# Kernel tuning notes

Hardware: AMD Instinct MI355X
Metric: run time of the kernel (lower is better)

The kernel has to match this reference:

```python
import jax, jax.numpy as jnp
import numpy as np

V, E, H = 50000, 128, 256  # vocab, embedding_size, hidden_size
S, B = 512, 64             # seq_len, batch (seq-first, torch LSTM default)


def setup_inputs() -> dict:
    key = jax.random.key(0)
    ks = jax.random.split(key, 10)
    u = 1.0 / np.sqrt(H)  # torch LSTM/Linear init bound

    def unif(k, sh):
        return jax.random.uniform(k, sh, jnp.float32, -u, u)

    emb = jax.random.normal(ks[0], (V, E), jnp.float32) * 0.02
    emb = emb.at[0].set(0.0)  # padding_idx=0

    inp = {
        "seq": jax.random.randint(ks[1], (S, B), 0, V),
        "emb": emb,
        # forward direction weights (gate order i,f,g,o like torch)
        "W_ih_f": unif(ks[2], (4 * H, E)),
        "W_hh_f": unif(ks[3], (4 * H, H)),
        "b_f": unif(ks[4], (4 * H,)),  # b_ih + b_hh fused (identical math)
        # reverse direction
        "W_ih_b": unif(ks[5], (4 * H, E)),
        "W_hh_b": unif(ks[6], (4 * H, H)),
        "b_b": unif(ks[7], (4 * H,)),
        # classification head over concatenated bi-directional features
        "W_out": unif(ks[8], (1, 2 * H)),
        "b_out": unif(ks[9], (1,)),
    }
    return inp


def _lstm_scan(xg, W_hh):
    """xg: [S,B,4H] precomputed input-gate projections; returns hidden seq [S,B,H]."""
    b = xg.shape[1]
    h0 = jnp.zeros((b, H), xg.dtype)
    c0 = jnp.zeros((b, H), xg.dtype)

    def step(carry, xg_t):
        h, c = carry
        gates = xg_t + h @ W_hh.T  # [B,4H]
        i, f, g, o = jnp.split(gates, 4, axis=-1)
        i = jax.nn.sigmoid(i)
        f = jax.nn.sigmoid(f)
        g = jnp.tanh(g)
        o = jax.nn.sigmoid(o)
        c = f * c + i * g
        h = o * jnp.tanh(c)
        return (h, c), h

    _, hs = jax.lax.scan(step, (h0, c0), xg)
    return hs


def reference(seq, emb, W_ih_f, W_hh_f, b_f, W_ih_b, W_hh_b, b_b, W_out, b_out):
    # embedding with padding_idx=0 (row 0 contributes zero)
    x = jnp.where((seq == 0)[..., None], 0.0, emb[seq])  # [S,B,E]

    xg_f = jnp.einsum("sbe,ge->sbg", x, W_ih_f) + b_f          # [S,B,4H]
    hs_f = _lstm_scan(xg_f, W_hh_f)                             # [S,B,H]

    xr = x[::-1]
    xg_b = jnp.einsum("sbe,ge->sbg", xr, W_ih_b) + b_b
    hs_b = _lstm_scan(xg_b, W_hh_b)[::-1]                       # [S,B,H]

    out = jnp.concatenate([hs_f, hs_b], axis=-1)                # [S,B,2H]
    last = out[-1]                                              # [B,2H]
    return jax.nn.sigmoid(last @ W_out.T + b_out)               # [B,1]
```

## Files before the change

kernel.cpp:

```cpp
#include <hip/hip_runtime.h>
#include <hip/hip_bf16.h>
#include <stdint.h>
#include <string.h>

#define S_LEN 512
#define NBATCH 64
#define EDIM 128
#define HDIM 256
#define GDIM 1024

#define WQ_SCALE 1024.0f
#define HQ_SCALE 127.0f
#define DEQ_SCALE (1.0f / 130048.0f)

typedef __attribute__((ext_vector_type(8))) short short8;
typedef __attribute__((ext_vector_type(4))) short short4v;
typedef __attribute__((ext_vector_type(4))) float float4v;
typedef __attribute__((ext_vector_type(4))) int int4v;

#define OFF_WHH8 0u
#define SZ_WHH8 (256u * 64u * 16u)
#define OFF_WIH (OFF_WHH8 + SZ_WHH8)
#define SZ_WIH (64u * 4u * 64u * 16u)
#define OFF_XG ((size_t)(OFF_WIH + SZ_WIH))
#define SZ_XG ((size_t)S_LEN * NBATCH * GDIM * 2)
#define OFF_HF (OFF_XG + SZ_XG)

__device__ __forceinline__ short f2bf(float f) {
    union { float f; unsigned u; } v;
    v.f = f;
    unsigned r = (v.u + 0x7fffu + ((v.u >> 16) & 1u)) >> 16;
    return (short)r;
}
__device__ __forceinline__ float bf2f(short s) {
    union { unsigned u; float f; } v;
    v.u = ((unsigned)(unsigned short)s) << 16;
    return v.f;
}
__device__ __forceinline__ float sigm(float x) {
    float e = __expf(-x);
    return __builtin_amdgcn_rcpf(1.0f + e);
}
__device__ __forceinline__ float tanh_(float x) {
    float e = __expf(2.0f * x);
    return 1.0f - 2.0f * __builtin_amdgcn_rcpf(e + 1.0f);
}

__global__ __launch_bounds__(256) void prep_frags(const float* __restrict__ src,
                                                  char* __restrict__ dst,
                                                  int K, int nchunks, int nfrags) {
    int id = blockIdx.x * blockDim.x + threadIdx.x;
    int lane = id & 63;
    int f = id >> 6;
    if (f >= nfrags) return;
    int tile = f / nchunks;
    int c = f - tile * nchunks;
    int row = tile * 16 + (lane & 15);
    int k0 = c * 32 + ((lane >> 4) * 8);
    const float* s = src + (size_t)row * K + k0;
    short8 pack;
#pragma unroll
    for (int j = 0; j < 8; ++j) pack[j] = f2bf(s[j]);
    *(short8*)(dst + ((size_t)f * 64 + lane) * 16) = pack;
}

__global__ __launch_bounds__(256) void prep_whh_i8(const float* __restrict__ src,
                                                   char* __restrict__ dst) {
    int id = blockIdx.x * blockDim.x + threadIdx.x;
    int lane = id & 63;
    int f = id >> 6;
    int tile = f >> 2, kc = f & 3;
    int row = tile * 16 + (lane & 15);
    int k0 = kc * 64 + ((lane >> 4) * 16);
    const float* s = src + (size_t)row * HDIM + k0;
    union { char b[16]; int4v v; } u;
#pragma unroll
    for (int b = 0; b < 16; ++b)
        u.b[b] = (char)(int)rintf(s[b] * WQ_SCALE);
    *(int4v*)(dst + ((size_t)f * 64 + lane) * 16) = u.v;
}

__global__ __launch_bounds__(256) void input_proj(const int* __restrict__ seq,
                                                  const float* __restrict__ emb,
                                                  const char* __restrict__ wih_frags,
                                                  const float* __restrict__ bias,
                                                  char* __restrict__ xg) {
    __shared__ __align__(16) short lx[4][16][136];
    int tid = threadIdx.x;
    int t0 = blockIdx.x * 4;
    int g = blockIdx.y;

    {
        int row = tid >> 2;
        int tt = row >> 4, m = row & 15;
        int k0 = (tid & 3) * 32;
        int v = seq[(t0 + tt) * NBATCH + g * 16 + m];
        const float* src = emb + (size_t)v * EDIM + k0;
        bool zero = (v == 0);
#pragma unroll
        for (int u = 0; u < 32; u += 4) {
            float4v f = *(const float4v*)(src + u);
            short4v p;
#pragma unroll
            for (int e = 0; e < 4; ++e) p[e] = zero ? (short)0 : f2bf(f[e]);
            *(short4v*)&lx[tt][m][k0 + u] = p;
        }
    }
    __syncthreads();

    int lane = tid & 63, w = tid >> 6;
    int ln = lane & 15, q = lane >> 4;

    short8 Bx[4][4];
#pragma unroll
    for (int tt = 0; tt < 4; ++tt)
#pragma unroll
        for (int c = 0; c < 4; ++c)
            Bx[tt][c] = *(const short8*)&lx[tt][ln][c * 32 + q * 8];

    for (int nt = 0; nt < 16; ++nt) {
        int tile = w * 16 + nt;
        short8 Aw[4];
#pragma unroll
        for (int c = 0; c < 4; ++c)
            Aw[c] = *(const short8*)(wih_frags + (((size_t)tile * 4 + c) * 64 + lane) * 16);
        float4v b4 = *(const float4v*)(bias + tile * 16 + q * 4);
#pragma unroll
        for (int tt = 0; tt < 4; ++tt) {
            float4v acc = b4;
#pragma unroll
            for (int c = 0; c < 4; ++c)
                acc = __builtin_amdgcn_mfma_f32_16x16x32_bf16(Aw[c], Bx[tt][c], acc, 0, 0, 0);
            short4v p;
#pragma unroll
            for (int r = 0; r < 4; ++r) p[r] = f2bf(acc[r]);
            size_t off = ((size_t)(t0 + tt) * NBATCH + g * 16 + ln) * GDIM + tile * 16 + q * 4;
            *(short4v*)(xg + off * 2) = p;
        }
    }
}

__global__ __launch_bounds__(1024, 4) void lstm_scan(const char* __restrict__ whh8,
                                                     const char* __restrict__ xg,
                                                     float* __restrict__ hf_out) {
    __shared__ __align__(16) char hls[2][16][272];
    __shared__ __align__(16) int scr[16][16 * 20];
    int tid = threadIdx.x;
    int lane = tid & 63, w = tid >> 6;
    int ln = lane & 15, q = lane >> 4;
    int bg = blockIdx.x;

    int4v Wfr[4][4];
#pragma unroll
    for (int blk = 0; blk < 4; ++blk) {
        int tile = 16 * blk + w;
#pragma unroll
        for (int kc = 0; kc < 4; ++kc)
            Wfr[blk][kc] = *(const int4v*)(whh8 + (((size_t)(tile * 4 + kc)) * 64 + lane) * 16);
    }

    {
        int* hp = (int*)&hls[0][0][0];
        for (int i = tid; i < (2 * 16 * 272) / 4; i += 1024) hp[i] = 0;
    }

    const char* hrd = &hls[0][0][0];
    char* hwr = &hls[1][0][0];
    int hoff_rd = ln * 272 + q * 16;

    int b = ln & 3;
    int rr = ln >> 2;
    int j = w * 16 + q * 4 + rr;
    int hoff_wr = b * 272 + j;
    int* swr = &scr[w][0] + (q * 4 + ln) * 20;
    const int* srd = &scr[w][0] + (q * 4 + b) * 20 + rr;

    float cst = 0.0f;

    const char* xgp = xg + (((size_t)(bg * 4 + b) * GDIM + j) * 2);
    const size_t tstep = (size_t)NBATCH * GDIM * 2;

    unsigned short xq[4];
#pragma unroll
    for (int blk = 0; blk < 4; ++blk)
        xq[blk] = *(const unsigned short*)(xgp + blk * 512);

    __syncthreads();

    for (int t = 0; t < S_LEN; ++t) {
        int4v Bh[4];
#pragma unroll
        for (int kc = 0; kc < 4; ++kc)
            Bh[kc] = *(const int4v*)(hrd + hoff_rd + kc * 64);

        float xgf[4];
#pragma unroll
        for (int blk = 0; blk < 4; ++blk) xgf[blk] = bf2f((short)xq[blk]);
        xgp += tstep;
        if (t != S_LEN - 1) {
#pragma unroll
            for (int blk = 0; blk < 4; ++blk)
                xq[blk] = *(const unsigned short*)(xgp + blk * 512);
        }

        int4v a[4];
#pragma unroll
        for (int blk = 0; blk < 4; ++blk) a[blk] = (int4v){0, 0, 0, 0};
#pragma unroll
        for (int kc = 0; kc < 4; ++kc)
#pragma unroll
            for (int blk = 0; blk < 4; ++blk)
                a[blk] = __builtin_amdgcn_mfma_i32_16x16x64_i8(Wfr[blk][kc], Bh[kc], a[blk], 0, 0, 0);

        if (ln < 4) {
#pragma unroll
            for (int blk = 0; blk < 4; ++blk)
                *(int4v*)(swr + blk * 4) = a[blk];
        }
        float gi = fmaf((float)srd[0], DEQ_SCALE, xgf[0]);
        float gf = fmaf((float)srd[4], DEQ_SCALE, xgf[1]);
        float gg = fmaf((float)srd[8], DEQ_SCALE, xgf[2]);
        float go = fmaf((float)srd[12], DEQ_SCALE, xgf[3]);

        float iv = sigm(gi);
        float fv = sigm(gf);
        float gv = tanh_(gg);
        float ov = sigm(go);
        float cv = fv * cst + iv * gv;
        cst = cv;
        float hv = ov * tanh_(cv);

        int hq = (int)rintf(hv * HQ_SCALE);
        hwr[hoff_wr] = (char)hq;

        if (t == S_LEN - 1)
            hf_out[((size_t)(bg * 4 + b)) * HDIM + j] = hv;

        const char* tr = hrd; hrd = hwr; hwr = (char*)tr;
        __syncthreads();
    }
}

__global__ __launch_bounds__(256) void tail_kernel(const int* __restrict__ seq,
                                                   const float* __restrict__ emb,
                                                   const float* __restrict__ wih_b,
                                                   const float* __restrict__ b_b,
                                                   const float* __restrict__ wout,
                                                   const float* __restrict__ b_out,
                                                   const float* __restrict__ hf,
                                                   float* __restrict__ out) {
    __shared__ float xs[EDIM];
    __shared__ float red[4];
    int b = blockIdx.x, tid = threadIdx.x;
    if (tid < EDIM) {
        int v = seq[(S_LEN - 1) * NBATCH + b];
        xs[tid] = (v == 0) ? 0.0f : emb[(size_t)v * EDIM + tid];
    }
    __syncthreads();

    int j = tid;
    float si = b_b[j], sg = b_b[2 * HDIM + j], so = b_b[3 * HDIM + j];
    const float* wi = wih_b + (size_t)j * EDIM;
    const float* wg = wih_b + (size_t)(2 * HDIM + j) * EDIM;
    const float* wo = wih_b + (size_t)(3 * HDIM + j) * EDIM;
#pragma unroll 8
    for (int k = 0; k < EDIM; k += 4) {
        float4v x4 = *(const float4v*)&xs[k];
        float4v a = *(const float4v*)(wi + k);
        float4v c = *(const float4v*)(wg + k);
        float4v d = *(const float4v*)(wo + k);
#pragma unroll
        for (int e = 0; e < 4; ++e) {
            si += a[e] * x4[e];
            sg += c[e] * x4[e];
            so += d[e] * x4[e];
        }
    }
    float cc = sigm(si) * tanh_(sg);
    float hb = sigm(so) * tanh_(cc);
    float partial = hf[(size_t)b * HDIM + j] * wout[j] + hb * wout[HDIM + j];

    float val = partial;
#pragma unroll
    for (int off = 32; off > 0; off >>= 1) val += __shfl_down(val, off, 64);
    int lane = tid & 63, wv = tid >> 6;
    if (lane == 0) red[wv] = val;
    __syncthreads();
    if (tid == 0) out[b] = sigm(red[0] + red[1] + red[2] + red[3] + b_out[0]);
}

extern "C" void kernel_launch(void* const* d_in, const int* in_sizes, int n_in,
                              void* d_out, int out_size, void* d_ws, size_t ws_size,
                              hipStream_t stream) {
    const int* seq = (const int*)d_in[0];
    const float* emb = (const float*)d_in[1];
    const float* Wih_f = (const float*)d_in[2];
    const float* Whh_f = (const float*)d_in[3];
    const float* b_f = (const float*)d_in[4];
    const float* Wih_b = (const float*)d_in[5];
    const float* b_b = (const float*)d_in[7];
    const float* Wout = (const float*)d_in[8];
    const float* b_out = (const float*)d_in[9];
    float* out = (float*)d_out;
    char* ws = (char*)d_ws;

    prep_whh_i8<<<dim3(64), 256, 0, stream>>>(Whh_f, ws + OFF_WHH8);
    prep_frags<<<dim3(64), 256, 0, stream>>>(Wih_f, ws + OFF_WIH, EDIM, 4, 64 * 4);
    input_proj<<<dim3(S_LEN / 4, 4), 256, 0, stream>>>(seq, emb, ws + OFF_WIH, b_f, ws + OFF_XG);
    lstm_scan<<<dim3(16), 1024, 0, stream>>>(ws + OFF_WHH8, ws + OFF_XG, (float*)(ws + OFF_HF));
    tail_kernel<<<dim3(NBATCH), 256, 0, stream>>>(seq, emb, Wih_b, b_b, Wout, b_out,
                                                  (const float*)(ws + OFF_HF), out);
}
```

Baseline: 696.0 us.

## Fuse input projection, LSTM scan and tail into one flag-synchronized kernel

Merges the input projection, the recurrent scan and the classification tail into a single launch. Blocks 16 and above compute the input-gate projections per 4-step chunk and publish them through release atomics on per-chunk flags, while the 16 scan blocks poll those flags so the recurrence can start before all projections finish. The two prep kernels are also combined and the tail reduction moves into the scan blocks, removing launches and the hf round-trip. The design depends on the producer blocks being scheduled alongside the scan blocks, and it adds spin-wait latency at each chunk boundary.

```diff
diff --git a/kernel.cpp b/kernel.cpp
--- a/kernel.cpp
+++ b/kernel.cpp
@@ -24,7 +24,7 @@
 #define SZ_WIH (64u * 4u * 64u * 16u)
 #define OFF_XG ((size_t)(OFF_WIH + SZ_WIH))
 #define SZ_XG ((size_t)S_LEN * NBATCH * GDIM * 2)
-#define OFF_HF (OFF_XG + SZ_XG)
+#define OFF_FLAGS (OFF_XG + SZ_XG)
 
 __device__ __forceinline__ short f2bf(float f) {
     union { float f; unsigned u; } v;
@@ -46,108 +46,118 @@
     return 1.0f - 2.0f * __builtin_amdgcn_rcpf(e + 1.0f);
 }
 
-__global__ __launch_bounds__(256) void prep_frags(const float* __restrict__ src,
-                                                  char* __restrict__ dst,
-                                                  int K, int nchunks, int nfrags) {
-    int id = blockIdx.x * blockDim.x + threadIdx.x;
-    int lane = id & 63;
-    int f = id >> 6;
-    if (f >= nfrags) return;
-    int tile = f / nchunks;
-    int c = f - tile * nchunks;
-    int row = tile * 16 + (lane & 15);
-    int k0 = c * 32 + ((lane >> 4) * 8);
-    const float* s = src + (size_t)row * K + k0;
-    short8 pack;
-#pragma unroll
-    for (int j = 0; j < 8; ++j) pack[j] = f2bf(s[j]);
-    *(short8*)(dst + ((size_t)f * 64 + lane) * 16) = pack;
-}
-
-__global__ __launch_bounds__(256) void prep_whh_i8(const float* __restrict__ src,
-                                                   char* __restrict__ dst) {
-    int id = blockIdx.x * blockDim.x + threadIdx.x;
-    int lane = id & 63;
-    int f = id >> 6;
-    int tile = f >> 2, kc = f & 3;
-    int row = tile * 16 + (lane & 15);
-    int k0 = kc * 64 + ((lane >> 4) * 16);
-    const float* s = src + (size_t)row * HDIM + k0;
-    union { char b[16]; int4v v; } u;
-#pragma unroll
-    for (int b = 0; b < 16; ++b)
-        u.b[b] = (char)(int)rintf(s[b] * WQ_SCALE);
-    *(int4v*)(dst + ((size_t)f * 64 + lane) * 16) = u.v;
-}
-
-__global__ __launch_bounds__(256) void input_proj(const int* __restrict__ seq,
-                                                  const float* __restrict__ emb,
-                                                  const char* __restrict__ wih_frags,
-                                                  const float* __restrict__ bias,
-                                                  char* __restrict__ xg) {
-    __shared__ __align__(16) short lx[4][16][136];
+__global__ __launch_bounds__(256) void prep_all(const float* __restrict__ Whh,
+                                                const float* __restrict__ Wih,
+                                                char* __restrict__ dstW,
+                                                char* __restrict__ dstI,
+                                                int* __restrict__ flags) {
     int tid = threadIdx.x;
-    int t0 = blockIdx.x * 4;
-    int g = blockIdx.y;
-
-    {
-        int row = tid >> 2;
-        int tt = row >> 4, m = row & 15;
-        int k0 = (tid & 3) * 32;
-        int v = seq[(t0 + tt) * NBATCH + g * 16 + m];
-        const float* src = emb + (size_t)v * EDIM + k0;
-        bool zero = (v == 0);
-#pragma unroll
-        for (int u = 0; u < 32; u += 4) {
-            float4v f = *(const float4v*)(src + u);
-            short4v p;
-#pragma unroll
-            for (int e = 0; e < 4; ++e) p[e] = zero ? (short)0 : f2bf(f[e]);
-            *(short4v*)&lx[tt][m][k0 + u] = p;
-        }
-    }
-    __syncthreads();
-
-    int lane = tid & 63, w = tid >> 6;
-    int ln = lane & 15, q = lane >> 4;
-
-    short8 Bx[4][4];
-#pragma unroll
-    for (int tt = 0; tt < 4; ++tt)
-#pragma unroll
-        for (int c = 0; c < 4; ++c)
-            Bx[tt][c] = *(const short8*)&lx[tt][ln][c * 32 + q * 8];
-
-    for (int nt = 0; nt < 16; ++nt) {
-        int tile = w * 16 + nt;
-        short8 Aw[4];
-#pragma unroll
-        for (int c = 0; c < 4; ++c)
-            Aw[c] = *(const short8*)(wih_frags + (((size_t)tile * 4 + c) * 64 + lane) * 16);
-        float4v b4 = *(const float4v*)(bias + tile * 16 + q * 4);
-#pragma unroll
-        for (int tt = 0; tt < 4; ++tt) {
-            float4v acc = b4;
-#pragma unroll
-            for (int c = 0; c < 4; ++c)
-                acc = __builtin_amdgcn_mfma_f32_16x16x32_bf16(Aw[c], Bx[tt][c], acc, 0, 0, 0);
-            short4v p;
-#pragma unroll
-            for (int r = 0; r < 4; ++r) p[r] = f2bf(acc[r]);
-            size_t off = ((size_t)(t0 + tt) * NBATCH + g * 16 + ln) * GDIM + tile * 16 + q * 4;
-            *(short4v*)(xg + off * 2) = p;
-        }
-    }
-}
-
-__global__ __launch_bounds__(1024, 4) void lstm_scan(const char* __restrict__ whh8,
-                                                     const char* __restrict__ xg,
-                                                     float* __restrict__ hf_out) {
+    if (blockIdx.x == 0 && tid < 128) flags[tid] = 0;
+    if (blockIdx.x < 64) {
+        int id = blockIdx.x * 256 + tid;
+        int lane = id & 63;
+        int f = id >> 6;
+        int tile = f >> 2, kc = f & 3;
+        int row = tile * 16 + (lane & 15);
+        int k0 = kc * 64 + ((lane >> 4) * 16);
+        const float* s = Whh + (size_t)row * HDIM + k0;
+        union { char b[16]; int4v v; } u;
+#pragma unroll
+        for (int b = 0; b < 16; ++b)
+            u.b[b] = (char)(int)rintf(s[b] * WQ_SCALE);
+        *(int4v*)(dstW + ((size_t)f * 64 + lane) * 16) = u.v;
+    } else {
+        int id = (blockIdx.x - 64) * 256 + tid;
+        int lane = id & 63;
+        int f = id >> 6;
+        int tile = f >> 2, c = f & 3;
+        int row = tile * 16 + (lane & 15);
+        int k0 = c * 32 + ((lane >> 4) * 8);
+        const float* s = Wih + (size_t)row * EDIM + k0;
+        short8 pack;
+#pragma unroll
+        for (int jj = 0; jj < 8; ++jj) pack[jj] = f2bf(s[jj]);
+        *(short8*)(dstI + ((size_t)f * 64 + lane) * 16) = pack;
+    }
+}
+
+__global__ __launch_bounds__(1024, 4) void lstm_mega(
+    const int* __restrict__ seq, const float* __restrict__ emb,
+    const char* __restrict__ whh8, const char* __restrict__ wih_frags,
+    const float* __restrict__ b_f, char* __restrict__ xg, int* __restrict__ flags,
+    const float* __restrict__ wih_b, const float* __restrict__ b_b,
+    const float* __restrict__ wout, const float* __restrict__ b_out,
+    float* __restrict__ out) {
     __shared__ __align__(16) char hls[2][16][272];
     __shared__ __align__(16) int scr[16][16 * 20];
+    __shared__ __align__(16) short lx[4][16][136];
+    __shared__ __align__(16) float xs2[4][132];
+    __shared__ float redf[16][4];
+    __shared__ float accB[4];
+
     int tid = threadIdx.x;
     int lane = tid & 63, w = tid >> 6;
     int ln = lane & 15, q = lane >> 4;
+
+    if (blockIdx.x >= 16) {
+        int i = blockIdx.x - 16;
+        int c = i >> 2, g = i & 3;
+        int t0 = c * 4;
+        {
+            int row = tid >> 4;
+            int tt = row >> 4, m = row & 15;
+            int kk = (tid & 15) * 8;
+            int v = seq[(t0 + tt) * NBATCH + g * 16 + m];
+            const float* src = emb + (size_t)v * EDIM + kk;
+            bool zero = (v == 0);
+            float4v f0 = *(const float4v*)(src);
+            float4v f1 = *(const float4v*)(src + 4);
+            short8 p;
+#pragma unroll
+            for (int e = 0; e < 4; ++e) {
+                p[e] = zero ? (short)0 : f2bf(f0[e]);
+                p[4 + e] = zero ? (short)0 : f2bf(f1[e]);
+            }
+            *(short8*)&lx[tt][m][kk] = p;
+        }
+        __syncthreads();
+
+        short8 Bx[4][4];
+#pragma unroll
+        for (int tt = 0; tt < 4; ++tt)
+#pragma unroll
+            for (int cc = 0; cc < 4; ++cc)
+                Bx[tt][cc] = *(const short8*)&lx[tt][ln][cc * 32 + q * 8];
+
+#pragma unroll
+        for (int nt = 0; nt < 4; ++nt) {
+            int tile = w * 4 + nt;
+            short8 Aw[4];
+#pragma unroll
+            for (int cc = 0; cc < 4; ++cc)
+                Aw[cc] = *(const short8*)(wih_frags + (((size_t)tile * 4 + cc) * 64 + lane) * 16);
+            float4v b4 = *(const float4v*)(b_f + tile * 16 + q * 4);
+#pragma unroll
+            for (int tt = 0; tt < 4; ++tt) {
+                float4v acc = b4;
+#pragma unroll
+                for (int cc = 0; cc < 4; ++cc)
+                    acc = __builtin_amdgcn_mfma_f32_16x16x32_bf16(Aw[cc], Bx[tt][cc], acc, 0, 0, 0);
+                short4v p;
+#pragma unroll
+                for (int r = 0; r < 4; ++r) p[r] = f2bf(acc[r]);
+                size_t off = ((size_t)(t0 + tt) * NBATCH + g * 16 + ln) * GDIM + tile * 16 + q * 4;
+                *(short4v*)(xg + off * 2) = p;
+            }
+        }
+        __syncthreads();
+        if (tid == 0) {
+            __threadfence();
+            __hip_atomic_fetch_add(&flags[c], 1, __ATOMIC_RELEASE, __HIP_MEMORY_SCOPE_AGENT);
+        }
+        return;
+    }
+
     int bg = blockIdx.x;
 
     int4v Wfr[4][4];
@@ -161,7 +171,7 @@
 
     {
         int* hp = (int*)&hls[0][0][0];
-        for (int i = tid; i < (2 * 16 * 272) / 4; i += 1024) hp[i] = 0;
+        for (int ii = tid; ii < (2 * 16 * 272) / 4; ii += 1024) hp[ii] = 0;
     }
 
     const char* hrd = &hls[0][0][0];
@@ -176,31 +186,38 @@
     const int* srd = &scr[w][0] + (q * 4 + b) * 20 + rr;
 
     float cst = 0.0f;
+    float hlast = 0.0f;
 
     const char* xgp = xg + (((size_t)(bg * 4 + b) * GDIM + j) * 2);
     const size_t tstep = (size_t)NBATCH * GDIM * 2;
 
-    unsigned short xq[4];
-#pragma unroll
-    for (int blk = 0; blk < 4; ++blk)
-        xq[blk] = *(const unsigned short*)(xgp + blk * 512);
-
+    if (tid == 0)
+        while (__hip_atomic_load(&flags[0], __ATOMIC_ACQUIRE, __HIP_MEMORY_SCOPE_AGENT) < 4) {}
     __syncthreads();
 
+    unsigned short xq[4], xq2[4];
     for (int t = 0; t < S_LEN; ++t) {
+        if ((t & 3) == 0) {
+#pragma unroll
+            for (int blk = 0; blk < 4; ++blk)
+                xq[blk] = *(const unsigned short*)(xgp + blk * 512);
+        }
+        int fv = 4;
+        bool bnd = ((t & 3) == 3) && (t + 1 < S_LEN);
+        if (bnd && tid == 0)
+            fv = __hip_atomic_load(&flags[(t + 1) >> 2], __ATOMIC_ACQUIRE, __HIP_MEMORY_SCOPE_AGENT);
+
         int4v Bh[4];
 #pragma unroll
         for (int kc = 0; kc < 4; ++kc)
             Bh[kc] = *(const int4v*)(hrd + hoff_rd + kc * 64);
 
-        float xgf[4];
-#pragma unroll
-        for (int blk = 0; blk < 4; ++blk) xgf[blk] = bf2f((short)xq[blk]);
+        bool pf2 = (((t + 1) & 3) != 0) && (t + 1 < S_LEN);
         xgp += tstep;
-        if (t != S_LEN - 1) {
+        if (pf2) {
 #pragma unroll
             for (int blk = 0; blk < 4; ++blk)
-                xq[blk] = *(const unsigned short*)(xgp + blk * 512);
+                xq2[blk] = *(const unsigned short*)(xgp + blk * 512);
         }
 
         int4v a[4];
@@ -217,76 +234,79 @@
             for (int blk = 0; blk < 4; ++blk)
                 *(int4v*)(swr + blk * 4) = a[blk];
         }
-        float gi = fmaf((float)srd[0], DEQ_SCALE, xgf[0]);
-        float gf = fmaf((float)srd[4], DEQ_SCALE, xgf[1]);
-        float gg = fmaf((float)srd[8], DEQ_SCALE, xgf[2]);
-        float go = fmaf((float)srd[12], DEQ_SCALE, xgf[3]);
+        float gi = fmaf((float)srd[0], DEQ_SCALE, bf2f((short)xq[0]));
+        float gf = fmaf((float)srd[4], DEQ_SCALE, bf2f((short)xq[1]));
+        float gg = fmaf((float)srd[8], DEQ_SCALE, bf2f((short)xq[2]));
+        float go = fmaf((float)srd[12], DEQ_SCALE, bf2f((short)xq[3]));
 
         float iv = sigm(gi);
-        float fv = sigm(gf);
+        float fvv = sigm(gf);
         float gv = tanh_(gg);
         float ov = sigm(go);
-        float cv = fv * cst + iv * gv;
+        float cv = fvv * cst + iv * gv;
         cst = cv;
         float hv = ov * tanh_(cv);
 
         int hq = (int)rintf(hv * HQ_SCALE);
         hwr[hoff_wr] = (char)hq;
-
-        if (t == S_LEN - 1)
-            hf_out[((size_t)(bg * 4 + b)) * HDIM + j] = hv;
+        if (t == S_LEN - 1) hlast = hv;
+
+        if (pf2) {
+#pragma unroll
+            for (int blk = 0; blk < 4; ++blk) xq[blk] = xq2[blk];
+        }
+        if (bnd && tid == 0)
+            while (fv < 4)
+                fv = __hip_atomic_load(&flags[(t + 1) >> 2], __ATOMIC_ACQUIRE, __HIP_MEMORY_SCOPE_AGENT);
 
         const char* tr = hrd; hrd = hwr; hwr = (char*)tr;
         __syncthreads();
     }
-}
-
-__global__ __launch_bounds__(256) void tail_kernel(const int* __restrict__ seq,
-                                                   const float* __restrict__ emb,
-                                                   const float* __restrict__ wih_b,
-                                                   const float* __restrict__ b_b,
-                                                   const float* __restrict__ wout,
-                                                   const float* __restrict__ b_out,
-                                                   const float* __restrict__ hf,
-                                                   float* __restrict__ out) {
-    __shared__ float xs[EDIM];
-    __shared__ float red[4];
-    int b = blockIdx.x, tid = threadIdx.x;
-    if (tid < EDIM) {
-        int v = seq[(S_LEN - 1) * NBATCH + b];
-        xs[tid] = (v == 0) ? 0.0f : emb[(size_t)v * EDIM + tid];
+
+    float pfd = hlast * wout[j];
+#pragma unroll
+    for (int m = 4; m <= 32; m <<= 1) pfd += __shfl_xor(pfd, m, 64);
+    if (lane < 4) redf[w][lane] = pfd;
+    if (tid < 4) accB[tid] = 0.0f;
+
+    int b2 = tid >> 8, j2 = tid & 255;
+    {
+        int vb = seq[(S_LEN - 1) * NBATCH + bg * 4 + b2];
+        if (j2 < EDIM) xs2[b2][j2] = (vb == 0) ? 0.0f : emb[(size_t)vb * EDIM + j2];
     }
     __syncthreads();
-
-    int j = tid;
-    float si = b_b[j], sg = b_b[2 * HDIM + j], so = b_b[3 * HDIM + j];
-    const float* wi = wih_b + (size_t)j * EDIM;
-    const float* wg = wih_b + (size_t)(2 * HDIM + j) * EDIM;
-    const float* wo = wih_b + (size_t)(3 * HDIM + j) * EDIM;
+    {
+        float si = b_b[j2], sg = b_b[2 * HDIM + j2], so = b_b[3 * HDIM + j2];
+        const float* wi = wih_b + (size_t)j2 * EDIM;
+        const float* wg = wih_b + (size_t)(2 * HDIM + j2) * EDIM;
+        const float* wo = wih_b + (size_t)(3 * HDIM + j2) * EDIM;
 #pragma unroll 8
-    for (int k = 0; k < EDIM; k += 4) {
-        float4v x4 = *(const float4v*)&xs[k];
-        float4v a = *(const float4v*)(wi + k);
-        float4v c = *(const float4v*)(wg + k);
-        float4v d = *(const float4v*)(wo + k);
-#pragma unroll
-        for (int e = 0; e < 4; ++e) {
-            si += a[e] * x4[e];
-            sg += c[e] * x4[e];
-            so += d[e] * x4[e];
-        }
-    }
-    float cc = sigm(si) * tanh_(sg);
-    float hb = sigm(so) * tanh_(cc);
-    float partial = hf[(size_t)b * HDIM + j] * wout[j] + hb * wout[HDIM + j];
-
-    float val = partial;
-#pragma unroll
-    for (int off = 32; off > 0; off >>= 1) val += __shfl_down(val, off, 64);
-    int lane = tid & 63, wv = tid >> 6;
-    if (lane == 0) red[wv] = val;
+        for (int k = 0; k < EDIM; k += 4) {
+            float4v x4 = *(const float4v*)&xs2[b2][k];
+            float4v aa = *(const float4v*)(wi + k);
+            float4v cc4 = *(const float4v*)(wg + k);
+            float4v dd = *(const float4v*)(wo + k);
+#pragma unroll
+            for (int e = 0; e < 4; ++e) {
+                si += aa[e] * x4[e];
+                sg += cc4[e] * x4[e];
+                so += dd[e] * x4[e];
+            }
+        }
+        float ccv = sigm(si) * tanh_(sg);
+        float hb = sigm(so) * tanh_(ccv);
+        float pb = hb * wout[HDIM + j2];
+#pragma unroll
+        for (int m = 1; m <= 32; m <<= 1) pb += __shfl_xor(pb, m, 64);
+        if (lane == 0) atomicAdd(&accB[b2], pb);
+    }
     __syncthreads();
-    if (tid == 0) out[b] = sigm(red[0] + red[1] + red[2] + red[3] + b_out[0]);
+    if (tid < 4) {
+        float s = accB[tid] + b_out[0];
+#pragma unroll
+        for (int w2 = 0; w2 < 16; ++w2) s += redf[w2][tid];
+        out[bg * 4 + tid] = sigm(s);
+    }
 }
 
 extern "C" void kernel_launch(void* const* d_in, const int* in_sizes, int n_in,
@@ -303,11 +323,10 @@
     const float* b_out = (const float*)d_in[9];
     float* out = (float*)d_out;
     char* ws = (char*)d_ws;
-
-    prep_whh_i8<<<dim3(64), 256, 0, stream>>>(Whh_f, ws + OFF_WHH8);
-    prep_frags<<<dim3(64), 256, 0, stream>>>(Wih_f, ws + OFF_WIH, EDIM, 4, 64 * 4);
-    input_proj<<<dim3(S_LEN / 4, 4), 256, 0, stream>>>(seq, emb, ws + OFF_WIH, b_f, ws + OFF_XG);
-    lstm_scan<<<dim3(16), 1024, 0, stream>>>(ws + OFF_WHH8, ws + OFF_XG, (float*)(ws + OFF_HF));
-    tail_kernel<<<dim3(NBATCH), 256, 0, stream>>>(seq, emb, Wih_b, b_b, Wout, b_out,
-                                                  (const float*)(ws + OFF_HF), out);
-}
+    int* flags = (int*)(ws + OFF_FLAGS);
+
+    prep_all<<<dim3(128), 256, 0, stream>>>(Whh_f, Wih_f, ws + OFF_WHH8, ws + OFF_WIH, flags);
+    lstm_mega<<<dim3(528), 1024, 0, stream>>>(seq, emb, ws + OFF_WHH8, ws + OFF_WIH,
+                                              b_f, ws + OFF_XG, flags,
+                                              Wih_b, b_b, Wout, b_out, out);
+}
```

Result: slower. 824.3 us (+18.4%).
